# Optimization experiments

Measured on AMD Instinct MI355X. Metric: run time of the kernel, lower is better.

## Reference

```python
import jax, jax.numpy as jnp
import numpy as np

N_INPUTS = 64
N_OUTPUTS = 64
N_OPS = 8  # ('none','linear','power_two','power_three','exp','ln','reciprocal','sin')
BATCH = 65536
TEMP = 1.0


def setup_inputs() -> dict:
    key = jax.random.key(0)
    k1, k2, k3 = jax.random.split(key, 3)
    # shift inputs into (0.5, 1.5) so ln / reciprocal are well-behaved
    x = jax.random.uniform(k1, (BATCH, N_INPUTS), dtype=jnp.float32) + 0.5
    alphas = 0.001 * jax.random.normal(k2, (N_INPUTS, N_OUTPUTS, N_OPS), dtype=jnp.float32)
    coeffs = jax.random.normal(k3, (N_INPUTS, N_OUTPUTS, N_OPS), dtype=jnp.float32)
    return {"x": x, "alphas": alphas, "coeffs": coeffs}


def _primitives(x):
    # x: [B, I] -> [B, I, N_OPS], one channel per primitive op
    return jnp.stack(
        [
            jnp.zeros_like(x),   # none
            x,                   # linear
            x * x,               # power_two
            x * x * x,           # power_three
            jnp.exp(x),          # exp
            jnp.log(x),          # ln
            1.0 / x,             # reciprocal
            jnp.sin(x),          # sin
        ],
        axis=-1,
    )


def reference(x, alphas, coeffs):
    # softmax gating over primitives (non-discrete, non-gumbel branch)
    gates = jax.nn.softmax(alphas / TEMP, axis=-1)        # [I, J, K]
    prims = _primitives(x)                                # [B, I, K]
    # operation_outputs[b,i,j] = sum_k gates[i,j,k] * coeffs[i,j,k] * prims[b,i,k]
    # layer_output[b,j] = sum_i operation_outputs[b,i,j]
    w = gates * coeffs                                    # [I, J, K]
    out = jnp.einsum("bik,ijk->bj", prims, w)            # [B, J]
    return out
```

## Files before the change

### kernel.cpp

```cpp
#include <hip/hip_runtime.h>
#include <hip/hip_bf16.h>
#include <stdint.h>


typedef __bf16 bf16x8 __attribute__((ext_vector_type(8)));
typedef float f32x4 __attribute__((ext_vector_type(4)));

typedef __attribute__((address_space(1))) void gvoid;
typedef __attribute__((address_space(3))) void lvoid;

__device__ __forceinline__ void async16(const void* g, void* l) {
    __builtin_amdgcn_global_load_lds((gvoid*)g, (lvoid*)l, 16, 0, 0);
}

__global__ void build_w(const float* __restrict__ alphas,
                        const float* __restrict__ coeffs,
                        __bf16* __restrict__ w2) {
    int gid = blockIdx.x * blockDim.x + threadIdx.x;
    int i = gid >> 6;
    int n = gid & 63;
    const float* a = alphas + gid * 8;
    const float* c = coeffs + gid * 8;

    float av[8], mx = -1e30f;
#pragma unroll
    for (int k = 0; k < 8; ++k) { av[k] = a[k]; mx = fmaxf(mx, av[k]); }
    float e[8], s = 0.f;
#pragma unroll
    for (int k = 0; k < 8; ++k) { e[k] = __expf(av[k] - mx); s += e[k]; }
    float inv = 1.0f / s;

    bf16x8 w;
#pragma unroll
    for (int k = 0; k < 8; ++k) w[k] = (__bf16)(e[k] * inv * c[k]);

    int cc = i >> 2, q = i & 3, t = n >> 4, nl = n & 15;
    int pos = ((cc * 4 + t) * 64 + q * 16 + nl) * 8;
    *(bf16x8*)(w2 + pos) = w;
}

__global__ __launch_bounds__(256) void darts_main(const float* __restrict__ x,
                                                  const __bf16* __restrict__ w2,
                                                  float* __restrict__ out) {
    __shared__ __bf16 wlds[32768];
    __shared__ float  xs[4096];

    const int tid  = threadIdx.x;
    const int lane = tid & 63;
    const int wv   = tid >> 6;

#pragma unroll
    for (int it = 0; it < 16; ++it) {
        async16((const char*)w2 + (it * 256 + tid) * 16,
                (char*)wlds + it * 4096 + wv * 1024);
    }

    const int m  = lane & 15;
    const int q  = lane >> 4;

    for (int tile = blockIdx.x; tile < 1024; tile += gridDim.x) {
#pragma unroll
        for (int it = 0; it < 4; ++it) {
            async16((const char*)x + tile * 16384 + (it * 256 + tid) * 16,
                    (char*)xs + it * 4096 + wv * 1024);
        }
        __syncthreads();

        f32x4 acc0 = {0.f, 0.f, 0.f, 0.f};
        f32x4 acc1 = {0.f, 0.f, 0.f, 0.f};
        f32x4 acc2 = {0.f, 0.f, 0.f, 0.f};
        f32x4 acc3 = {0.f, 0.f, 0.f, 0.f};

        const float* xrow = xs + (wv * 16 + m) * 64;

#pragma unroll
        for (int c = 0; c < 16; ++c) {
            float xv = xrow[c * 4 + q];
            float x2 = xv * xv;
            bf16x8 a;
            a[0] = (__bf16)0.0f;
            a[1] = (__bf16)xv;
            a[2] = (__bf16)x2;
            a[3] = (__bf16)(x2 * xv);
            a[4] = (__bf16)__expf(xv);
            a[5] = (__bf16)__logf(xv);
            a[6] = (__bf16)__builtin_amdgcn_rcpf(xv);
            a[7] = (__bf16)__sinf(xv);

            const __bf16* bbase = wlds + (c * 4) * 512 + lane * 8;
            bf16x8 b0 = *(const bf16x8*)(bbase);
            bf16x8 b1 = *(const bf16x8*)(bbase + 512);
            bf16x8 b2 = *(const bf16x8*)(bbase + 1024);
            bf16x8 b3 = *(const bf16x8*)(bbase + 1536);
            acc0 = __builtin_amdgcn_mfma_f32_16x16x32_bf16(a, b0, acc0, 0, 0, 0);
            acc1 = __builtin_amdgcn_mfma_f32_16x16x32_bf16(a, b1, acc1, 0, 0, 0);
            acc2 = __builtin_amdgcn_mfma_f32_16x16x32_bf16(a, b2, acc2, 0, 0, 0);
            acc3 = __builtin_amdgcn_mfma_f32_16x16x32_bf16(a, b3, acc3, 0, 0, 0);
        }

        __syncthreads();

        float* orow = out + (tile * 64 + wv * 16 + q * 4) * 64 + m;
#pragma unroll
        for (int r = 0; r < 4; ++r) {
            orow[r * 64 + 0]  = acc0[r];
            orow[r * 64 + 16] = acc1[r];
            orow[r * 64 + 32] = acc2[r];
            orow[r * 64 + 48] = acc3[r];
        }
    }
}

extern "C" void kernel_launch(void* const* d_in, const int* in_sizes, int n_in,
                              void* d_out, int out_size, void* d_ws, size_t ws_size,
                              hipStream_t stream) {
    const float* x      = (const float*)d_in[0];
    const float* alphas = (const float*)d_in[1];
    const float* coeffs = (const float*)d_in[2];
    float* out = (float*)d_out;
    __bf16* w2 = (__bf16*)d_ws;

    build_w<<<16, 256, 0, stream>>>(alphas, coeffs, w2);
    darts_main<<<512, 256, 0, stream>>>(x, w2, out);
}
```

Before: 80.10 us.

## Load x directly into registers with one 128-row tile per block

Drops the persistent tile loop and the x staging buffer in LDS. Each 512-thread block now handles a single 128-row tile, and each lane loads 16 contiguous x values straight into registers with vector loads. The weight layout is permuted so every lane's K-chunk is 16 consecutive input features, which keeps the x reads contiguous. The goal is to remove LDS round trips and per-tile barriers for x, and to raise occupancy. The cost is that the weight tile in LDS is reloaded once per block instead of once per persistent block.

```diff
diff --git a/kernel.cpp b/kernel.cpp
--- a/kernel.cpp
+++ b/kernel.cpp
@@ -34,80 +34,77 @@
 #pragma unroll
     for (int k = 0; k < 8; ++k) w[k] = (__bf16)(e[k] * inv * c[k]);
 
-    int cc = i >> 2, q = i & 3, t = n >> 4, nl = n & 15;
+    int q = i >> 4, cc = i & 15, t = n >> 4, nl = n & 15;
     int pos = ((cc * 4 + t) * 64 + q * 16 + nl) * 8;
     *(bf16x8*)(w2 + pos) = w;
 }
 
-__global__ __launch_bounds__(256) void darts_main(const float* __restrict__ x,
-                                                  const __bf16* __restrict__ w2,
-                                                  float* __restrict__ out) {
+__global__ __launch_bounds__(512, 4) void darts_main(const float* __restrict__ x,
+                                                     const __bf16* __restrict__ w2,
+                                                     float* __restrict__ out) {
     __shared__ __bf16 wlds[32768];
-    __shared__ float  xs[4096];
 
     const int tid  = threadIdx.x;
     const int lane = tid & 63;
     const int wv   = tid >> 6;
+    const int m    = lane & 15;
+    const int q    = lane >> 4;
+
+    const int row = blockIdx.x * 128 + wv * 16 + m;
+    const float* xp = x + row * 64 + q * 16;
+    f32x4 xr0 = *(const f32x4*)(xp + 0);
+    f32x4 xr1 = *(const f32x4*)(xp + 4);
+    f32x4 xr2 = *(const f32x4*)(xp + 8);
+    f32x4 xr3 = *(const f32x4*)(xp + 12);
 
 #pragma unroll
-    for (int it = 0; it < 16; ++it) {
-        async16((const char*)w2 + (it * 256 + tid) * 16,
-                (char*)wlds + it * 4096 + wv * 1024);
+    for (int it = 0; it < 8; ++it) {
+        async16((const char*)w2 + (it * 512 + tid) * 16,
+                (char*)wlds + it * 8192 + wv * 1024);
+    }
+    __syncthreads();
+
+    float xa[16];
+#pragma unroll
+    for (int c = 0; c < 4; ++c) { xa[c] = xr0[c]; xa[4+c] = xr1[c]; xa[8+c] = xr2[c]; xa[12+c] = xr3[c]; }
+
+    f32x4 acc0 = {0.f, 0.f, 0.f, 0.f};
+    f32x4 acc1 = {0.f, 0.f, 0.f, 0.f};
+    f32x4 acc2 = {0.f, 0.f, 0.f, 0.f};
+    f32x4 acc3 = {0.f, 0.f, 0.f, 0.f};
+
+#pragma unroll
+    for (int c = 0; c < 16; ++c) {
+        float xv = xa[c];
+        float x2 = xv * xv;
+        bf16x8 a;
+        a[0] = (__bf16)0.0f;
+        a[1] = (__bf16)xv;
+        a[2] = (__bf16)x2;
+        a[3] = (__bf16)(x2 * xv);
+        a[4] = (__bf16)__expf(xv);
+        a[5] = (__bf16)__logf(xv);
+        a[6] = (__bf16)__builtin_amdgcn_rcpf(xv);
+        a[7] = (__bf16)__sinf(xv);
+
+        const __bf16* bb = wlds + c * 2048 + lane * 8;
+        bf16x8 b0 = *(const bf16x8*)(bb);
+        bf16x8 b1 = *(const bf16x8*)(bb + 512);
+        bf16x8 b2 = *(const bf16x8*)(bb + 1024);
+        bf16x8 b3 = *(const bf16x8*)(bb + 1536);
+        acc0 = __builtin_amdgcn_mfma_f32_16x16x32_bf16(a, b0, acc0, 0, 0, 0);
+        acc1 = __builtin_amdgcn_mfma_f32_16x16x32_bf16(a, b1, acc1, 0, 0, 0);
+        acc2 = __builtin_amdgcn_mfma_f32_16x16x32_bf16(a, b2, acc2, 0, 0, 0);
+        acc3 = __builtin_amdgcn_mfma_f32_16x16x32_bf16(a, b3, acc3, 0, 0, 0);
     }
 
-    const int m  = lane & 15;
-    const int q  = lane >> 4;
-
-    for (int tile = blockIdx.x; tile < 1024; tile += gridDim.x) {
+    float* orow = out + (blockIdx.x * 128 + wv * 16 + q * 4) * 64 + m;
 #pragma unroll
-        for (int it = 0; it < 4; ++it) {
-            async16((const char*)x + tile * 16384 + (it * 256 + tid) * 16,
-                    (char*)xs + it * 4096 + wv * 1024);
-        }
-        __syncthreads();
-
-        f32x4 acc0 = {0.f, 0.f, 0.f, 0.f};
-        f32x4 acc1 = {0.f, 0.f, 0.f, 0.f};
-        f32x4 acc2 = {0.f, 0.f, 0.f, 0.f};
-        f32x4 acc3 = {0.f, 0.f, 0.f, 0.f};
-
-        const float* xrow = xs + (wv * 16 + m) * 64;
-
-#pragma unroll
-        for (int c = 0; c < 16; ++c) {
-            float xv = xrow[c * 4 + q];
-            float x2 = xv * xv;
-            bf16x8 a;
-            a[0] = (__bf16)0.0f;
-            a[1] = (__bf16)xv;
-            a[2] = (__bf16)x2;
-            a[3] = (__bf16)(x2 * xv);
-            a[4] = (__bf16)__expf(xv);
-            a[5] = (__bf16)__logf(xv);
-            a[6] = (__bf16)__builtin_amdgcn_rcpf(xv);
-            a[7] = (__bf16)__sinf(xv);
-
-            const __bf16* bbase = wlds + (c * 4) * 512 + lane * 8;
-            bf16x8 b0 = *(const bf16x8*)(bbase);
-            bf16x8 b1 = *(const bf16x8*)(bbase + 512);
-            bf16x8 b2 = *(const bf16x8*)(bbase + 1024);
-            bf16x8 b3 = *(const bf16x8*)(bbase + 1536);
-            acc0 = __builtin_amdgcn_mfma_f32_16x16x32_bf16(a, b0, acc0, 0, 0, 0);
-            acc1 = __builtin_amdgcn_mfma_f32_16x16x32_bf16(a, b1, acc1, 0, 0, 0);
-            acc2 = __builtin_amdgcn_mfma_f32_16x16x32_bf16(a, b2, acc2, 0, 0, 0);
-            acc3 = __builtin_amdgcn_mfma_f32_16x16x32_bf16(a, b3, acc3, 0, 0, 0);
-        }
-
-        __syncthreads();
-
-        float* orow = out + (tile * 64 + wv * 16 + q * 4) * 64 + m;
-#pragma unroll
-        for (int r = 0; r < 4; ++r) {
-            orow[r * 64 + 0]  = acc0[r];
-            orow[r * 64 + 16] = acc1[r];
-            orow[r * 64 + 32] = acc2[r];
-            orow[r * 64 + 48] = acc3[r];
-        }
+    for (int r = 0; r < 4; ++r) {
+        orow[r * 64 + 0]  = acc0[r];
+        orow[r * 64 + 16] = acc1[r];
+        orow[r * 64 + 32] = acc2[r];
+        orow[r * 64 + 48] = acc3[r];
     }
 }
 
@@ -121,5 +118,5 @@
     __bf16* w2 = (__bf16*)d_ws;
 
     build_w<<<16, 256, 0, stream>>>(alphas, coeffs, w2);
-    darts_main<<<512, 256, 0, stream>>>(x, w2, out);
+    darts_main<<<512, 512, 0, stream>>>(x, w2, out);
 }
```

Result: no change. 78.73 us (-1.7%).
